# Performance work log

Hardware: AMD Instinct MI355X
Metric: run time of the kernel (lower is better)

Reference implementation:

```python
import jax, jax.numpy as jnp
import numpy as np

D_IN = 128      # NODE/EDGE_EMBEDDING_SIZE
FC_HID = 512    # FC_HIDDEN_SIZE
FEAT = 256      # GNN_FEAT_SIZE
N1 = 2000; E1 = 2000; N2 = 2000; E2 = 2000
GNN_LAYERS = 3
ALPHA = 200.0   # NORM_ALPHA
BS_ITERS = 10   # BS_ITER_NUM
BS_EPS = 1e-4   # BS_EPSILON


def _l2norm(x, axis=-1, eps=1e-12):
    # torch F.normalize(p=2): x / max(||x||, eps)
    n = jnp.sqrt(jnp.sum(x * x, axis=axis, keepdims=True))
    return x / jnp.maximum(n, eps)


def _pairwise_sim(x, y):
    # s = 1 - cdist(x,y,p=2)/max  on batched [B,N,D],[B,M,D]
    x2 = jnp.sum(x * x, axis=-1)[:, :, None]
    y2 = jnp.sum(y * y, axis=-1)[:, None, :]
    d2 = jnp.maximum(x2 + y2 - 2.0 * jnp.einsum('bnd,bmd->bnm', x, y), 0.0)
    dist = jnp.sqrt(d2)
    return 1.0 - dist / jnp.max(dist)


def _gconv(A, x, w_a, b_a, w_u, b_u):
    # A: [B,N,N]; F.normalize(A, p=1, dim=-2) = column L1 normalization
    An = A / jnp.maximum(jnp.sum(jnp.abs(A), axis=-2, keepdims=True), 1e-12)
    ax = jax.nn.relu(x @ w_a + b_a)
    ux = jax.nn.relu(x @ w_u + b_u)
    return jnp.einsum('bnm,bmd->bnd', An, ax) + ux


def _affinity(X, Y, A):
    S = (A + A.T) * 0.5
    return jnp.einsum('bnd,de,bme->bnm', X, S, Y)


def _sinkhorn(s, n1, n2):
    # nrows/ncols equal full dims in Net.forward, so masks are full blocks.
    NT1, NT2 = s.shape[1], s.shape[2]
    r = jnp.arange(NT1)[:, None]
    c = jnp.arange(NT2)[None, :]
    block = ((r < n1) & (c < n2)) | ((r >= n1) & (c >= n2))
    s = (s + BS_EPS) * block[None].astype(s.dtype)
    for i in range(BS_ITERS):
        if i % 2 == 1:
            s = s / jnp.sum(s, axis=2, keepdims=True)  # row normalization
        else:
            s = s / jnp.sum(s, axis=1, keepdims=True)  # column normalization
    return s


def setup_inputs() -> dict:
    key = jax.random.key(0)
    ks = jax.random.split(key, 22)
    f32 = jnp.float32
    def lin_w(k, din, dout):
        return jax.random.uniform(k, (din, dout), dtype=f32,
                                  minval=-1.0, maxval=1.0) / np.sqrt(din)
    stdv = 1.0 / np.sqrt(FEAT)
    inp = {
        'emb1': jax.random.normal(ks[0], (1, N1, D_IN), dtype=f32),
        'emb2': jax.random.normal(ks[1], (1, N2, D_IN), dtype=f32),
        'edge_emb1': jax.random.normal(ks[2], (1, E1, D_IN), dtype=f32),
        'edge_emb2': jax.random.normal(ks[3], (1, E2, D_IN), dtype=f32),
        'Aidx_src': jax.random.uniform(ks[4], (1, N1 + E1, N1 + E1), dtype=f32),
        'Aidx_tgt': jax.random.uniform(ks[5], (1, N2 + E2, N2 + E2), dtype=f32),
        'fc1n_w': lin_w(ks[6], D_IN, FC_HID), 'fc1n_b': jnp.zeros((FC_HID,), f32),
        'fc2n_w': lin_w(ks[7], FC_HID, FEAT), 'fc2n_b': jnp.zeros((FEAT,), f32),
        'fc1e_w': lin_w(ks[8], D_IN, FC_HID), 'fc1e_b': jnp.zeros((FC_HID,), f32),
        'fc2e_w': lin_w(ks[9], FC_HID, FEAT), 'fc2e_b': jnp.zeros((FEAT,), f32),
        'gnn_a_w': jnp.stack([lin_w(k, FEAT, FEAT) for k in jax.random.split(ks[10], GNN_LAYERS)]),
        'gnn_a_b': jnp.zeros((GNN_LAYERS, FEAT), f32),
        'gnn_u_w': jnp.stack([lin_w(k, FEAT, FEAT) for k in jax.random.split(ks[11], GNN_LAYERS)]),
        'gnn_u_b': jnp.zeros((GNN_LAYERS, FEAT), f32),
        'aff_A': jax.random.uniform(ks[12], (GNN_LAYERS, FEAT, FEAT), dtype=f32,
                                    minval=-stdv, maxval=stdv) + jnp.eye(FEAT, dtype=f32),
        'cg_w': lin_w(ks[13], 2 * FEAT, FEAT), 'cg_b': jnp.zeros((FEAT,), f32),
    }
    return inp


def reference(emb1, emb2, edge_emb1, edge_emb2, Aidx_src, Aidx_tgt,
              fc1n_w, fc1n_b, fc2n_w, fc2n_b, fc1e_w, fc1e_b, fc2e_w, fc2e_b,
              gnn_a_w, gnn_a_b, gnn_u_w, gnn_u_b, aff_A, cg_w, cg_b):
    # node embeddings
    h1 = jax.nn.relu(emb1[0] @ fc1n_w + fc1n_b)
    e1n = _l2norm(h1 @ fc2n_w + fc2n_b)[None]            # [1,N1,FEAT]
    h2 = jax.nn.relu(emb2[0] @ fc1n_w + fc1n_b)
    e2n = _l2norm(h2 @ fc2n_w + fc2n_b)[None]            # [1,N2,FEAT]
    Kp = _pairwise_sim(e1n, e2n)
    # edge embeddings
    g1 = jax.nn.relu(edge_emb1[0] @ fc1e_w + fc1e_b)
    e1e = jax.nn.sigmoid(g1 @ fc2e_w + fc2e_b)[None]     # [1,E1,FEAT]
    g2 = jax.nn.relu(edge_emb2[0] @ fc1e_w + fc1e_b)
    e2e = jax.nn.sigmoid(g2 @ fc2e_w + fc2e_b)[None]     # [1,E2,FEAT]
    Ke = _pairwise_sim(e1e, e2e)

    n1, n2 = e1n.shape[1], e2n.shape[1]
    x1 = jnp.concatenate([e1n, e1e], axis=1)             # [1,N1+E1,FEAT]
    x2 = jnp.concatenate([e2n, e2e], axis=1)
    NT1, NT2 = x1.shape[1], x2.shape[1]

    s = None
    for i in range(GNN_LAYERS):
        x1 = _l2norm(_gconv(Aidx_src, x1, gnn_a_w[i], gnn_a_b[i], gnn_u_w[i], gnn_u_b[i]))
        x2 = _l2norm(_gconv(Aidx_tgt, x2, gnn_a_w[i], gnn_a_b[i], gnn_u_w[i], gnn_u_b[i]))
        s = jnp.zeros((1, NT1, NT2), dtype=x1.dtype)
        s = s.at[:, :n1, :n2].set(_affinity(x1[:, :n1], x2[:, :n2], aff_A[i]))
        s = s.at[:, n1:, n2:].set(_affinity(x1[:, n1:], x2[:, n2:], aff_A[i]))
        s = jax.nn.softmax(ALPHA * s, axis=-1)           # Norm layer
        s = _sinkhorn(s, n1, n2)
        if i == GNN_LAYERS - 2:
            x1n = jnp.concatenate([x1, jnp.einsum('bnm,bmd->bnd', s, x2)], axis=-1) @ cg_w + cg_b
            x2n = jnp.concatenate([x2, jnp.einsum('bnm,bnd->bmd', s, x1)], axis=-1) @ cg_w + cg_b
            x1, x2 = x1n, x2n
    return (s, Kp, Ke)
```

## Files before the change

kernel.cpp:

```cpp
#include <hip/hip_runtime.h>
#include <hip/hip_bf16.h>
#include <math.h>
#include <stdint.h>

typedef __hip_bfloat16 bf16;

#define NN 2000
#define NT 4000
#define FEAT 256
#define FC_HID 512
#define D_IN 128
#define ALPHA_C 200.0f
#define BS_EPS_C 1e-4f
#define SABLK 4000000

__device__ __forceinline__ float ldv_dt(const void* p, size_t i, int dt)
{
    return dt ? __bfloat162float(((const bf16*)p)[i]) : ((const float*)p)[i];
}
__device__ __forceinline__ void stv_dt(void* p, size_t i, float v, int dt)
{
    if (dt) ((bf16*)p)[i] = __float2bfloat16(v);
    else    ((float*)p)[i] = v;
}
__device__ __forceinline__ short f2bf(float f)
{
    bf16 h = __float2bfloat16(f);
    short s; __builtin_memcpy(&s, &h, 2); return s;
}
__device__ __forceinline__ float bfbits2f(uint32_t u16)
{
    uint32_t x = u16 << 16; float f; __builtin_memcpy(&f, &x, 4); return f;
}

__device__ __forceinline__ void swizzle_tiles(int& tx, int& ty, int& tz)
{
    int gx = gridDim.x, gy = gridDim.y, gz = gridDim.z;
    int nwg = gx * gy * gz;
    int flat = ((int)blockIdx.z * gy + (int)blockIdx.y) * gx + (int)blockIdx.x;
    int q = nwg >> 3, r = nwg & 7;
    int xcd = flat & 7, s = flat >> 3;
    int mn = xcd < r ? xcd : r;
    int g = xcd * q + mn + s;
    tx = g % gx;
    int gg = g / gx;
    ty = gg % gy;
    tz = gg / gy;
}

__global__ __launch_bounds__(256) void detect_kernel(const uint32_t* __restrict__ emb,
                                                     int* __restrict__ flag)
{
    int tid = threadIdx.x;
    int cnt = 0;
    for (int i = tid; i < 1024; i += 256) {
        uint32_t e = (emb[i] >> 7) & 0xFF;
        if (e >= 0x30 && e <= 0x44) cnt++;
    }
    for (int o = 32; o; o >>= 1) cnt += __shfl_down(cnt, o);
    __shared__ int red[4];
    if ((tid & 63) == 0) red[tid >> 6] = cnt;
    __syncthreads();
    if (tid == 0) *flag = (red[0] + red[1] + red[2] + red[3] > 512) ? 1 : 0;
}

__global__ void telemetry_kernel(uint32_t* out, uint32_t pattern) { out[0] = pattern; }

// ... 136 lines not shown
                int m = t >> 2;
                int gm = m0 + m;
                short loc[8];
#pragma unroll
                for (int j = 0; j < 8; ++j) {
                    int gkj = gk + j;
                    float v = (hv && gm < M && gkj < K)
                                  ? ((const float*)A)[a_off + (size_t)gkj * lda + gm] : 0.f;
                    loc[j] = f2bf(v);
                }
                *(bf16x8*)&Als[t >> 2][h * LDST + kk] = *(bf16x8*)loc;
            }
            {
                int n = t >> 2;
                int gn = n0 + n;
                short* dst = &Bls[n][h * LDST + kk];
                if (hv && gn < N && gk + 8 <= K) {
                    if (bet) {
                        *(uint4*)dst = *(const uint4*)((const ushort*)B + b_off + (size_t)gn * ldb + gk);
                    } else {
                        const float* p = (const float*)B + b_off + (size_t)gn * ldb + gk;
                        float4 r0 = *(const float4*)p, r1 = *(const float4*)(p + 4);
                        short loc[8];
                        loc[0] = f2bf(r0.x); loc[1] = f2bf(r0.y);
                        loc[2] = f2bf(r0.z); loc[3] = f2bf(r0.w);
                        loc[4] = f2bf(r1.x); loc[5] = f2bf(r1.y);
                        loc[6] = f2bf(r1.z); loc[7] = f2bf(r1.w);
                        *(bf16x8*)dst = *(bf16x8*)loc;
                    }
                } else {
                    short loc[8];
#pragma unroll
                    for (int j = 0; j < 8; ++j) {
                        float v = (hv && gn < N && gk + j < K)
                                      ? ldv_dt(B, b_off + (size_t)gn * ldb + gk + j, bet) : 0.f;
                        loc[j] = f2bf(v);
                    }
                    *(bf16x8*)dst = *(bf16x8*)loc;
                }
            }
        }
        __syncthreads();
#pragma unroll
        for (int h = 0; h < 2; ++h) {
            bf16x8 a = *(const bf16x8*)&Als[w * 16 + l16][h * LDST + quad * 8];
#pragma unroll
            for (int fb = 0; fb < 4; ++fb) {
                bf16x8 b = *(const bf16x8*)&Bls[fb * 16 + l16][h * LDST + quad * 8];
                acc[fb] = __builtin_amdgcn_mfma_f32_16x16x32_bf16(a, b, acc[fb], 0, 0, 0);
            }
        }
        __syncthreads();
    }
    const bool atom = (nz > 1);
#pragma unroll
    for (int fb = 0; fb < 4; ++fb) {
        int gc = n0 + fb * 16 + l16;
        if (gc >= N) continue;
        float bv = (!atom && bias) ? ldv_dt(bias, bias_off + gc, bdt) : 0.f;
#pragma unroll
        for (int r = 0; r < 4; ++r) {
            int gr = m0 + w * 16 + quad * 4 + r;
            if (gr >= M) continue;
            float v = acc[fb][r];
            if (atom) {
                if (rowscale) v *= rowscale[gr];
                atomicAdd(&C[(size_t)gr * ldc + gc], v);
            } else {
                v += bv;
                if (epi == 1) v = fmaxf(v, 0.f);
                else if (epi == 2) v = 1.f / (1.f + expf(-v));
                if (rowscale) v *= rowscale[gr];
                if (addsrc) v += addsrc[(size_t)gr * ldadd + gc];
                C[(size_t)gr * ldc + gc] = v;
            }
        }
    }
}

template <int ATR>
__global__ __launch_bounds__(256) void mfma_gemm2(
    const void* __restrict__ A0, const void* __restrict__ A1, int amode,
    const void* __restrict__ B, int bmode, size_t b_off0, size_t b_off1,
    float* __restrict__ C0, float* __restrict__ C1,
    int M, int N, int K, int lda, int ldb, int ldc,
    const float* __restrict__ rs0, const float* __restrict__ rs1,
    const int* __restrict__ dtp)
{
    __shared__ short Als[64][LDSROW];
    __shared__ short Bls[64][LDSROW];
    const int dtf = *dtp;
    const int aet = amode ? dtf : 0;
    const int bet = (bmode == 2) ? 1 : (bmode == 1 ? dtf : 0);
    const int t = threadIdx.x;
    int bx, by, bz;
    swizzle_tiles(bx, by, bz);
    const int tilesY = (M + 63) >> 6;
    const int half = (by >= tilesY) ? 1 : 0;
    const int m0 = (by - half * tilesY) * 64;
    const int n0 = bx * 64;
    const void* A = half ? A1 : A0;
    float* C = half ? C1 : C0;
    const size_t b_off = half ? b_off1 : b_off0;
    const float* rowscale = half ? rs1 : rs0;
    const int nz = gridDim.z;
    int zlo = 0, zhi = K;
    if (nz > 1) {
// ... 44 lines not shown
                int m = t >> 2;
                int gm = m0 + m;
                short loc[8];
#pragma unroll
                for (int j = 0; j < 8; ++j) {
                    int gkj = gk + j;
                    float v = (hv && gm < M && gkj < K)
                                  ? ((const float*)A)[(size_t)gkj * lda + gm] : 0.f;
                    loc[j] = f2bf(v);
                }
                *(bf16x8*)&Als[t >> 2][h * LDST + kk] = *(bf16x8*)loc;
            }
            {
                int n = t >> 2;
                int gn = n0 + n;
                short* dst = &Bls[n][h * LDST + kk];
                if (hv && gn < N && gk + 8 <= K) {
                    if (bet) {
                        *(uint4*)dst = *(const uint4*)((const ushort*)B + b_off + (size_t)gn * ldb + gk);
                    } else {
                        const float* p = (const float*)B + b_off + (size_t)gn * ldb + gk;
                        float4 r0 = *(const float4*)p, r1 = *(const float4*)(p + 4);
                        short loc[8];
                        loc[0] = f2bf(r0.x); loc[1] = f2bf(r0.y);
                        loc[2] = f2bf(r0.z); loc[3] = f2bf(r0.w);
                        loc[4] = f2bf(r1.x); loc[5] = f2bf(r1.y);
                        loc[6] = f2bf(r1.z); loc[7] = f2bf(r1.w);
                        *(bf16x8*)dst = *(bf16x8*)loc;
                    }
                } else {
                    short loc[8];
#pragma unroll
                    for (int j = 0; j < 8; ++j) {
                        float v = (hv && gn < N && gk + j < K)
                                      ? ldv_dt(B, b_off + (size_t)gn * ldb + gk + j, bet) : 0.f;
                        loc[j] = f2bf(v);
                    }
                    *(bf16x8*)dst = *(bf16x8*)loc;
                }
            }
        }
        __syncthreads();
#pragma unroll
        for (int h = 0; h < 2; ++h) {
            bf16x8 a = *(const bf16x8*)&Als[w * 16 + l16][h * LDST + quad * 8];
#pragma unroll
            for (int fb = 0; fb < 4; ++fb) {
                bf16x8 b = *(const bf16x8*)&Bls[fb * 16 + l16][h * LDST + quad * 8];
                acc[fb] = __builtin_amdgcn_mfma_f32_16x16x32_bf16(a, b, acc[fb], 0, 0, 0);
            }
        }
        __syncthreads();
    }
    const bool atom = (nz > 1);
#pragma unroll
    for (int fb = 0; fb < 4; ++fb) {
        int gc = n0 + fb * 16 + l16;
        if (gc >= N) continue;
#pragma unroll
        for (int r = 0; r < 4; ++r) {
            int gr = m0 + w * 16 + quad * 4 + r;
            if (gr >= M) continue;
            float v = acc[fb][r];
            if (rowscale) v *= rowscale[gr];
            if (atom) atomicAdd(&C[(size_t)gr * ldc + gc], v);
            else      C[(size_t)gr * ldc + gc] = v;
        }
    }
}

__global__ __launch_bounds__(256) void mfma_gemm_split(
    const float* __restrict__ A, const float* __restrict__ B, float* __restrict__ C,
    int M, int N, int K)
{
    __shared__ short Ahi[64][LDST];
    __shared__ short Alo[64][LDST];
    __shared__ short Bhi[64][LDST];
    __shared__ short Blo[64][LDST];
    const int t = threadIdx.x;
    int bx, by, bz;
    swizzle_tiles(bx, by, bz);
    const int m0 = by * 64;
    const int n0 = bx * 64;
    const int w = t >> 6, lane = t & 63, quad = lane >> 4, l16 = lane & 15;

    floatx4 acc[4] = {};

    for (int k0 = 0; k0 < K; k0 += 32) {
        {
            int r = t >> 2, kk = (t & 3) * 8;
            int gm = m0 + r, gk = k0 + kk;
            float v[8] = {};
            if (gm < M) {
                const float* p = A + (size_t)gm * K + gk;
                float4 r0 = *(const float4*)p, r1 = *(const float4*)(p + 4);
                v[0] = r0.x; v[1] = r0.y; v[2] = r0.z; v[3] = r0.w;
                v[4] = r1.x; v[5] = r1.y; v[6] = r1.z; v[7] = r1.w;
            }
            short lh[8], ll[8];
#pragma unroll
            for (int j = 0; j < 8; ++j) {
                short h = f2bf(v[j]);
                lh[j] = h;
                ll[j] = f2bf(v[j] - bfbits2f((uint32_t)(uint16_t)h));
            }
            *(bf16x8*)&Ahi[r][kk] = *(bf16x8*)lh;
            *(bf16x8*)&Alo[r][kk] = *(bf16x8*)ll;
        }
        {
            int r = t >> 2, kk = (t & 3) * 8;
            int gn = n0 + r, gk = k0 + kk;
            float v[8] = {};
            if (gn < N) {
                const float* p = B + (size_t)gn * K + gk;
                float4 r0 = *(const float4*)p, r1 = *(const float4*)(p + 4);
                v[0] = r0.x; v[1] = r0.y; v[2] = r0.z; v[3] = r0.w;
                v[4] = r1.x; v[5] = r1.y; v[6] = r1.z; v[7] = r1.w;
            }
            short lh[8], ll[8];
#pragma unroll
            for (int j = 0; j < 8; ++j) {
                short h = f2bf(v[j]);
                lh[j] = h;
                ll[j] = f2bf(v[j] - bfbits2f((uint32_t)(uint16_t)h));
            }
            *(bf16x8*)&Bhi[r][kk] = *(bf16x8*)lh;
            *(bf16x8*)&Blo[r][kk] = *(bf16x8*)ll;
        }
        __syncthreads();
        bf16x8 ah = *(const bf16x8*)&Ahi[w * 16 + l16][quad * 8];
        bf16x8 al = *(const bf16x8*)&Alo[w * 16 + l16][quad * 8];
#pragma unroll
        for (int fb = 0; fb < 4; ++fb) {
            bf16x8 bh = *(const bf16x8*)&Bhi[fb * 16 + l16][quad * 8];
            bf16x8 bl = *(const bf16x8*)&Blo[fb * 16 + l16][quad * 8];
            acc[fb] = __builtin_amdgcn_mfma_f32_16x16x32_bf16(ah, bh, acc[fb], 0, 0, 0);
            acc[fb] = __builtin_amdgcn_mfma_f32_16x16x32_bf16(al, bh, acc[fb], 0, 0, 0);
            acc[fb] = __builtin_amdgcn_mfma_f32_16x16x32_bf16(ah, bl, acc[fb], 0, 0, 0);
        }
        __syncthreads();
    }
#pragma unroll
    for (int fb = 0; fb < 4; ++fb) {
        int gc = n0 + fb * 16 + l16;
        if (gc >= N) continue;
#pragma unroll
        for (int r = 0; r < 4; ++r) {
            int gr = m0 + w * 16 + quad * 4 + r;
            if (gr >= M) continue;
            C[(size_t)gr * N + gc] = acc[fb][r];
        }
    }
}

__global__ __launch_bounds__(256) void mfma_mlp_split(
    const void* __restrict__ A, int amode,
    const short* __restrict__ Whi, const short* __restrict__ Wlo,
    float* __restrict__ C, int M, int N, int K, int ldc,
    const void* __restrict__ bias, int epi, const int* __restrict__ dtp)
{
    __shared__ short Ahi[64][LDST];
    __shared__ short Alo[64][LDST];
    __shared__ short Bh[64][LDST];
    __shared__ short Bl[64][LDST];
    const int dtf = *dtp;
    const int aet = amode ? dtf : 0;
    const int t = threadIdx.x;
    int bx, by, bz;
    swizzle_tiles(bx, by, bz);
    const int m0 = by * 64;
    const int n0 = bx * 64;
    const int w = t >> 6, lane = t & 63, quad = lane >> 4, l16 = lane & 15;

    floatx4 acc[4] = {};

    for (int k0 = 0; k0 < K; k0 += 32) {
        {
            int r = t >> 2, kk = (t & 3) * 8;
            int gm = m0 + r, gk = k0 + kk;
            float v[8] = {};
            if (gm < M) {
                if (aet) {
                    uint4 raw = *(const uint4*)((const ushort*)A + (size_t)gm * K + gk);
                    uint32_t uu[4] = {raw.x, raw.y, raw.z, raw.w};
#pragma unroll
                    for (int q = 0; q < 4; ++q) {
                        v[2 * q]     = bfbits2f(uu[q] & 0xFFFFu);
                        v[2 * q + 1] = bfbits2f(uu[q] >> 16);
                    }
                } else {
                    const float* p = (const float*)A + (size_t)gm * K + gk;
                    float4 r0 = *(const float4*)p, r1 = *(const float4*)(p + 4);
                    v[0] = r0.x; v[1] = r0.y; v[2] = r0.z; v[3] = r0.w;
                    v[4] = r1.x; v[5] = r1.y; v[6] = r1.z; v[7] = r1.w;
                }
            }
            short lh[8], ll[8];
#pragma unroll
            for (int j = 0; j < 8; ++j) {
                short h = f2bf(v[j]);
                lh[j] = h;
                ll[j] = f2bf(v[j] - bfbits2f((uint32_t)(uint16_t)h));
            }
            *(bf16x8*)&Ahi[r][kk] = *(bf16x8*)lh;
            *(bf16x8*)&Alo[r][kk] = *(bf16x8*)ll;
        }
        {
            int n = t >> 2, kk = (t & 3) * 8;
            int gn = n0 + n, gk = k0 + kk;
            if (gn < N) {
                *(uint4*)&Bh[n][kk] = *(const uint4*)&Whi[(size_t)gn * K + gk];
                *(uint4*)&Bl[n][kk] = *(const uint4*)&Wlo[(size_t)gn * K + gk];
            } else {
                short z[8] = {};
                *(bf16x8*)&Bh[n][kk] = *(bf16x8*)z;
                *(bf16x8*)&Bl[n][kk] = *(bf16x8*)z;
            }
        }
        __syncthreads();
        bf16x8 ah = *(const bf16x8*)&Ahi[w * 16 + l16][quad * 8];
        bf16x8 al = *(const bf16x8*)&Alo[w * 16 + l16][quad * 8];
#pragma unroll
        for (int fb = 0; fb < 4; ++fb) {
            bf16x8 bh = *(const bf16x8*)&Bh[fb * 16 + l16][quad * 8];
// ... 5 lines not shown
        __syncthreads();
    }
#pragma unroll
    for (int fb = 0; fb < 4; ++fb) {
        int gc = n0 + fb * 16 + l16;
        if (gc >= N) continue;
        float bv = bias ? ldv_dt(bias, gc, *dtp) : 0.f;
#pragma unroll
        for (int r = 0; r < 4; ++r) {
            int gr = m0 + w * 16 + quad * 4 + r;
            if (gr >= M) continue;
            float v = acc[fb][r] + bv;
            if (epi == 1) v = fmaxf(v, 0.f);
            else if (epi == 2) v = 1.f / (1.f + expf(-v));
            C[(size_t)gr * ldc + gc] = v;
        }
    }
}

__global__ void fill_kernel(float* p, float v, int n)
{
    int i = blockIdx.x * 256 + threadIdx.x;
    if (i < n) p[i] = v;
}

__global__ __launch_bounds__(256) void l2norm_kernel(const float* __restrict__ src,
                                                     int lds, float* __restrict__ dst)
{
    int row = blockIdx.x, tid = threadIdx.x;
    float v = src[(size_t)row * lds + tid];
    float s = v * v;
    for (int o = 32; o; o >>= 1) s += __shfl_down(s, o);
    __shared__ float red[4];
    if ((tid & 63) == 0) red[tid >> 6] = s;
    __syncthreads();
    float tot = red[0] + red[1] + red[2] + red[3];
    float scale = 1.f / fmaxf(sqrtf(tot), 1e-12f);
    dst[(size_t)row * FEAT + tid] = v * scale;
}

__global__ __launch_bounds__(256) void rownorm2_kernel(const float* __restrict__ src,
                                                       float* __restrict__ out)
{
    int row = blockIdx.x, tid = threadIdx.x;
    float v = src[(size_t)row * FEAT + tid];
    float s = v * v;
    for (int o = 32; o; o >>= 1) s += __shfl_down(s, o);
    __shared__ float red[4];
    if ((tid & 63) == 0) red[tid >> 6] = s;
    __syncthreads();
    if (tid == 0) out[row] = red[0] + red[1] + red[2] + red[3];
}

__global__ __launch_bounds__(256) void d2max_rows_kernel(const float* __restrict__ G,
                                                         const float* __restrict__ x2,
                                                         const float* __restrict__ y2,
                                                         float* __restrict__ rowmax)
{
    int i = blockIdx.x, tid = threadIdx.x;
    float xi = x2[i];
    const float* Gr = G + (size_t)i * NN;
    float m = 0.f;
    for (int j = tid; j < NN; j += 256)
        m = fmaxf(m, xi + y2[j] - 2.f * Gr[j]);
    for (int o = 32; o; o >>= 1) m = fmaxf(m, __shfl_down(m, o));
    __shared__ float red[4];
    if ((tid & 63) == 0) red[tid >> 6] = m;
    __syncthreads();
    if (tid == 0) rowmax[i] = fmaxf(fmaxf(red[0], red[1]), fmaxf(red[2], red[3]));
}

__global__ __launch_bounds__(256) void maxreduce_kernel(const float* __restrict__ rowmax,
                                                        float* __restrict__ gmax, int n)
{
    int tid = threadIdx.x;
    float m = 0.f;
    for (int i = tid; i < n; i += 256) m = fmaxf(m, rowmax[i]);
    for (int o = 32; o; o >>= 1) m = fmaxf(m, __shfl_down(m, o));
    __shared__ float red[4];
    if ((tid & 63) == 0) red[tid >> 6] = m;
    __syncthreads();
    if (tid == 0) *gmax = sqrtf(fmaxf(fmaxf(fmaxf(red[0], red[1]),
                                            fmaxf(red[2], red[3])), 0.f));
}

__global__ __launch_bounds__(256) void pw_out_kernel(void* __restrict__ out, size_t elem_off,
                                                     const float* __restrict__ G,
                                                     const float* __restrict__ x2,
                                                     const float* __restrict__ y2,
                                                     const float* __restrict__ gmax,
                                                     const int* __restrict__ dtp)
{
    int j = blockIdx.x * 256 + threadIdx.x;
    int i = blockIdx.y;
    if (j >= NN) return;
    float inv = 1.f / *gmax;
    float d2 = fmaxf(x2[i] + y2[j] - 2.f * G[(size_t)i * NN + j], 0.f);
    stv_dt(out, elem_off + (size_t)i * NN + j, 1.f - sqrtf(d2) * inv, *dtp);
}

__global__ __launch_bounds__(256) void colsum_kernel(const void* __restrict__ A0,
                                                     const void* __restrict__ A1,
                                                     float* __restrict__ out,
                                                     const int* __restrict__ dtp)
{
    const void* A = blockIdx.z ? A1 : A0;
    int dt = *dtp;
    int col = blockIdx.x * 256 + threadIdx.x;
    if (col >= NT) return;
    int r0 = blockIdx.y * 100;
    float s = 0.f;
#pragma unroll 4
    for (int r = r0; r < r0 + 100; ++r) s += fabsf(ldv_dt(A, (size_t)r * NT + col, dt));
    atomicAdd(&out[blockIdx.z * NT + col], s);
}

__global__ void recipclamp_kernel(float* p, int n)
{
    int i = blockIdx.x * 256 + threadIdx.x;
    if (i < n) p[i] = 1.f / fmaxf(p[i], 1e-12f);
}

__global__ __launch_bounds__(256) void symavg_kernel(const void* __restrict__ A,
                                                     size_t a_off,
                                                     float* __restrict__ S,
                                                     const int* __restrict__ dtp)
{
    int dt = *dtp;
    int i = blockIdx.x, j = threadIdx.x;
    S[i * 256 + j] = 0.5f * (ldv_dt(A, a_off + i * 256 + j, dt) +
                             ldv_dt(A, a_off + j * 256 + i, dt));
}

__global__ __launch_bounds__(256) void softmax_stats_kernel(const float* __restrict__ Sa,
                                                            float* __restrict__ ms,
                                                            float* __restrict__ dinv)
{
    int row = blockIdx.x, z = blockIdx.z, tid = threadIdx.x;
    const float* Srow = Sa + (size_t)z * SABLK + (size_t)row * NN;
    __shared__ float red[4];
    float m = 0.f;
    for (int j = tid; j < NN; j += 256) m = fmaxf(m, ALPHA_C * Srow[j]);
    for (int o = 32; o; o >>= 1) m = fmaxf(m, __shfl_down(m, o));
    if ((tid & 63) == 0) red[tid >> 6] = m;
    __syncthreads();
    m = fmaxf(fmaxf(red[0], red[1]), fmaxf(red[2], red[3]));
    __syncthreads();
    float s = 0.f;
    for (int j = tid; j < NN; j += 256) s += expf(ALPHA_C * Srow[j] - m);
    for (int o = 32; o; o >>= 1) s += __shfl_down(s, o);
// ... 64 lines not shown
}

__global__ __launch_bounds__(256) void writes_kernel(void* __restrict__ out,
                                                     const float* __restrict__ E,
                                                     const float* __restrict__ rvec,
                                                     const float* __restrict__ cvec,
                                                     const int* __restrict__ dtp)
{
    int i = blockIdx.x, tid = threadIdx.x;
    int dt = *dtp;
    int z = (i < NN) ? 0 : 1;
    int r = z ? i - NN : i;
    const float* Erow = E + (size_t)z * SABLK + (size_t)r * NN;
    float rv = rvec[i];
    for (int j = tid; j < NT; j += 256) {
        float v = 0.f;
        bool inblk = z ? (j >= NN) : (j < NN);
        if (inblk) {
            int jj = z ? (j - NN) : j;
            v = rv * Erow[jj] * cvec[j];
            if (!(v == v) || fabsf(v) > 1e30f) v = 0.f;
        }
        stv_dt(out, (size_t)i * NT + j, v, dt);
    }
}

extern "C" void kernel_launch(void* const* d_in, const int* in_sizes, int n_in,
                              void* d_out, int out_size, void* d_ws, size_t ws_size,
                              hipStream_t stream)
{
    (void)in_sizes; (void)n_in; (void)out_size;
    const void* emb1   = d_in[0];
    const void* emb2   = d_in[1];
    const void* eemb1  = d_in[2];
    const void* eemb2  = d_in[3];
    const void* Asrc   = d_in[4];
    const void* Atgt   = d_in[5];
    const void* fc1n_w = d_in[6];
    const void* fc1n_b = d_in[7];
    const void* fc2n_w = d_in[8];
    const void* fc2n_b = d_in[9];
    const void* fc1e_w = d_in[10];
    const void* fc1e_b = d_in[11];
    const void* fc2e_w = d_in[12];
    const void* fc2e_b = d_in[13];
    const void* gnn_a_w = d_in[14];
    const void* gnn_a_b = d_in[15];
    const void* gnn_u_w = d_in[16];
    const void* gnn_u_b = d_in[17];
    const void* aff_A  = d_in[18];
    const void* cg_w   = d_in[19];
    const void* cg_b   = d_in[20];

    const size_t KP_OFF = 16000000;
    const size_t KE_OFF = 20000000;

    const size_t NEED = 50808960;
    if (ws_size < NEED) {
        float tv = 10000.f + (float)(ws_size >> 20);
        bf16 tb = __float2bfloat16(tv);
        uint16_t tbits; __builtin_memcpy(&tbits, &tb, 2);
        uint32_t pattern = ((uint32_t)tbits << 16) | tbits;
        telemetry_kernel<<<1, 1, 0, stream>>>((uint32_t*)d_out, pattern);
        return;
    }
    char* Wb = (char*)d_ws;
    size_t off = 0;
    auto allocf = [&](size_t n) { float* p = (float*)(Wb + off); off += n * 4; return p; };
    float* x1     = allocf(1024000);
    float* x2     = allocf(1024000);
    float* ax     = allocf(1024000);
    float* ux     = allocf(1024000);
    float* XS     = allocf(512000);
    float* Ssym   = allocf(65536);
    float* colsum = allocf(8192);
    float* rn2a   = allocf(2048);
    float* rn2b   = allocf(2048);
    float* rvec   = allocf(4096);
    float* cvec   = allocf(4096);
    float* ms     = allocf(4096);
    float* dinv   = allocf(4096);
    float* gmax   = allocf(16);
    int*   dtp    = (int*)allocf(16);
    float* Sa     = allocf(8000000);
    float* G      = Sa;
    float* tmpx1  = Sa;
    float* tmpx2  = Sa + 1024000;
    float* h      = ax;
    float* partial = XS;
    float* XS2    = ax;
    short* wuT    = (short*)(Sa + 2100000);
    float* bias512 = Sa + 2200000;
    float* axu_b  = Sa + 2300000;
    short* axT_b  = (short*)(Sa + 6450000);
    short* cgT    = (short*)Ssym;
    short* XST    = (short*)XS;
    short* w1hiT = (short*)Sa;
    short* w1loT = w1hiT + FC_HID * D_IN;
    short* w2hiT = w1loT + FC_HID * D_IN;
    short* w2loT = w2hiT + FEAT * FC_HID;

    dim3 B(256);
    auto g2 = [](int M, int N) { return dim3((N + 63) / 64, (M + 63) / 64); };
    auto gb2 = [](int Mh, int N, int nz) {
        return dim3((N + 63) / 64, 2 * ((Mh + 63) / 64), nz);
    };
    auto gt = [](int R, int C) { return dim3((C + 63) / 64, (R + 63) / 64); };
    const float* NF = nullptr;
    const void* NV = nullptr;

    detect_kernel<<<1, B, 0, stream>>>((const uint32_t*)emb1, dtp);

    struct { const void* e; const void* w1; const void* b1; const void* w2;
             const void* b2; float* dst; int epi; } mlp[4] = {
        {emb1,  fc1n_w, fc1n_b, fc2n_w, fc2n_b, x1,          0},
        {emb2,  fc1n_w, fc1n_b, fc2n_w, fc2n_b, x2,          0},
        {eemb1, fc1e_w, fc1e_b, fc2e_w, fc2e_b, x1 + 512000, 2},
        {eemb2, fc1e_w, fc1e_b, fc2e_w, fc2e_b, x2 + 512000, 2},
    };
    for (int m = 0; m < 4; ++m) {
        if (m == 0 || m == 2) {
            transpose_split_kernel<<<gt(D_IN, FC_HID), B, 0, stream>>>(
                mlp[m].w1, 1, 0, w1hiT, w1loT, D_IN, FC_HID, dtp);
            transpose_split_kernel<<<gt(FC_HID, FEAT), B, 0, stream>>>(
                mlp[m].w2, 1, 0, w2hiT, w2loT, FC_HID, FEAT, dtp);
        }
        mfma_mlp_split<<<g2(NN, FC_HID), B, 0, stream>>>(
            mlp[m].e, 1, w1hiT, w1loT, h, NN, FC_HID, D_IN, FC_HID,
            mlp[m].b1, 1, dtp);
        mfma_mlp_split<<<g2(NN, FEAT), B, 0, stream>>>(
            h, 0, w2hiT, w2loT, mlp[m].dst, NN, FEAT, FC_HID, FEAT,
            mlp[m].b2, mlp[m].epi, dtp);
        if (mlp[m].epi == 0)
            l2norm_kernel<<<NN, B, 0, stream>>>(mlp[m].dst, FEAT, mlp[m].dst);
    }

    for (int e = 0; e < 2; ++e) {
        const float* a = e ? x1 + 512000 : x1;
        const float* b = e ? x2 + 512000 : x2;
        size_t oeo = e ? KE_OFF : KP_OFF;
        rownorm2_kernel<<<NN, B, 0, stream>>>(a, rn2a);
        rownorm2_kernel<<<NN, B, 0, stream>>>(b, rn2b);
        mfma_gemm_split<<<g2(NN, NN), B, 0, stream>>>(a, b, G, NN, NN, FEAT);
        d2max_rows_kernel<<<NN, B, 0, stream>>>(G, rn2a, rn2b, partial);
        maxreduce_kernel<<<1, B, 0, stream>>>(partial, gmax, NN);
        pw_out_kernel<<<dim3(8, NN), B, 0, stream>>>(d_out, oeo, G, rn2a, rn2b, gmax, dtp);
    }

    fill_kernel<<<(8192 + 255) / 256, B, 0, stream>>>(colsum, 0.f, 8192);
    colsum_kernel<<<dim3(16, 40, 2), B, 0, stream>>>(Asrc, Atgt, colsum, dtp);
    recipclamp_kernel<<<(8000 + 255) / 256, B, 0, stream>>>(colsum, 8000);

    float* src1 = x1;
    for (int i = 0; i < 3; ++i) {
        size_t wo = (size_t)i * 65536, bo = (size_t)i * 256;
        transpose_bf16_kernel<<<gt(256, 256), B, 0, stream>>>(
            gnn_a_w, 1, wo, wuT, 256, 256, 256, NF, dtp);
        transpose_bf16_kernel<<<gt(256, 256), B, 0, stream>>>(
            gnn_u_w, 1, wo, wuT + 65536, 256, 256, 256, NF, dtp);
        concat_bias_kernel<<<1, B, 0, stream>>>(gnn_a_b, gnn_u_b, bo, bias512, dtp);
        mfma_gemm<0><<<g2(2 * NT, 512), B, 0, stream>>>(
            src1, 0, 0, wuT, 2, 0, axu_b, 2 * NT, 512, FEAT, FEAT, FEAT, 512,
            bias512, 0, 0, NF, NF, 0, 1, dtp);
        transpose_bf16_kernel<<<gt(2 * NT, 256), B, 0, stream>>>(
            axu_b, 0, 0, axT_b, 2 * NT, 256, 512, colsum, dtp);
        mfma_gemm2<0><<<gb2(NT, FEAT, 8), B, 0, stream>>>(
            Asrc, Atgt, 1, axT_b, 2, 0, NT,
            axu_b + 256, axu_b + (size_t)NT * 512 + 256,
            NT, FEAT, NT, NT, 2 * NT, 512, NF, NF, dtp);
        l2norm_kernel<<<2 * NT, B, 0, stream>>>(axu_b + 256, 512, x1);
        src1 = x1;
        if (i >= 1) {
            symavg_kernel<<<256, B, 0, stream>>>(aff_A, (size_t)i * 65536, Ssym, dtp);
            mfma_gemm<0><<<g2(2 * NN, FEAT), B, 0, stream>>>(
                x1, 0, 0, Ssym, 0, 0, XS2, 2 * NN, FEAT, FEAT, FEAT, FEAT, FEAT,
                NV, 0, 0, NF, NF, 0, 0, dtp);
            mfma_gemm2<0><<<gb2(NN, NN, 1), B, 0, stream>>>(
                XS2, XS2 + 512000, 0, x2, 0, 0, 512000,
                Sa, Sa + SABLK, NN, NN, FEAT, FEAT, FEAT, NN, NF, NF, dtp);
            softmax_stats_kernel<<<dim3(NN, 1, 2), B, 0, stream>>>(Sa, ms, dinv);
            exp_transform_kernel<<<dim3(2, NN, 2), B, 0, stream>>>(Sa, ms, dinv);
            for (int t = 0; t < 10; ++t) {
                if ((t & 1) == 0) {
                    fill_kernel<<<16, B, 0, stream>>>(partial, 0.f, 4096);
                    colmv_partial_kernel<<<dim3(8, 40, 2), B, 0, stream>>>(
                        Sa, t == 0 ? NF : rvec, partial);
                    recip_vec_kernel<<<16, B, 0, stream>>>(partial, cvec, 4000);
                } else {
                    rowmv_kernel<<<dim3(NN, 1, 2), B, 0, stream>>>(Sa, cvec, rvec);
                }
            }
            if (i == 1) {
                fill_kernel<<<8000, B, 0, stream>>>(ax, 0.f, 2048000);
                transpose_bf16_kernel<<<gt(2 * NN, 256), B, 0, stream>>>(
                    x2, 0, 0, XST, 2 * NN, 256, 256, cvec, dtp);
                mfma_gemm2<0><<<gb2(NN, FEAT, 8), B, 0, stream>>>(
                    Sa, Sa + SABLK, 0, XST, 2, 0, NN,
                    ax, ax + 512000, NN, FEAT, NN, NN, 2 * NN, FEAT,
                    rvec, rvec + NN, dtp);
                transpose_bf16_kernel<<<gt(2 * NN, 256), B, 0, stream>>>(
                    x1, 0, 0, XST, 2 * NN, 256, 256, rvec, dtp);
                mfma_gemm2<1><<<gb2(NN, FEAT, 8), B, 0, stream>>>(
                    Sa, Sa + SABLK, 0, XST, 2, 0, NN,
                    ux, ux + 512000, NN, FEAT, NN, NN, 2 * NN, FEAT,
                    cvec, cvec + NN, dtp);
                transpose_bf16_kernel<<<gt(512, 256), B, 0, stream>>>(
                    cg_w, 1, 0, cgT, 512, 256, 256, NF, dtp);
                mfma_gemm<0><<<g2(2 * NT, FEAT), B, 0, stream>>>(
                    x1, 0, 0, cgT, 2, 0, tmpx1, 2 * NT, FEAT, FEAT, FEAT, 512, FEAT,
                    cg_b, 0, 1, NF, NF, 0, 0, dtp);
                mfma_gemm<0><<<g2(2 * NT, FEAT), B, 0, stream>>>(
                    ax, 0, 0, cgT, 2, 256, tmpx1, 2 * NT, FEAT, FEAT, FEAT, 512, FEAT,
                    NV, 0, 0, NF, tmpx1, FEAT, 0, dtp);
                src1 = tmpx1;
            }
            if (i == 2) {
                writes_kernel<<<NT, B, 0, stream>>>(d_out, Sa, rvec, cvec, dtp);
            }
        }
    }
}
```

Measured before the change: 1.425 ms.

## Use 128x128 MFMA tiles for aggregation GEMMs and batch paired preprocessing launches

Adds a 128x128-tile variant of the paired GEMM, with each wave computing a 64x64 sub-tile, and uses it for the large A·X aggregation and S·X cross-graph products. This raises data reuse per loaded LDS tile. It also merges the MLP and pairwise-similarity stages for the two graphs into single launches using a half/z index, which roughly halves the number of launches in the prologue. The larger tiles use more registers and produce fewer blocks, which could reduce occupancy.

After: 1.448 ms. No clear change (+1.6%).

```diff
diff --git a/kernel.cpp b/kernel.cpp
--- a/kernel.cpp
+++ b/kernel.cpp
@@ -13,6 +13,8 @@
 #define ALPHA_C 200.0f
 #define BS_EPS_C 1e-4f
 #define SABLK 4000000
+#define KP_OFF_C 16000000
+#define KE_OFF_C 20000000
 
 __device__ __forceinline__ float ldv_dt(const void* p, size_t i, int dt)
 {
@@ -255,7 +257,7 @@
         }
         __syncthreads();
     }
-    const bool atom = (nz > 1);
+    const bool atom = (gridDim.z > 1);
 #pragma unroll
     for (int fb = 0; fb < 4; ++fb) {
         int gc = n0 + fb * 16 + l16;
@@ -406,7 +408,7 @@
         }
         __syncthreads();
     }
-    const bool atom = (nz > 1);
+    const bool atom = (gridDim.z > 1);
 #pragma unroll
     for (int fb = 0; fb < 4; ++fb) {
         int gc = n0 + fb * 16 + l16;
@@ -423,8 +425,157 @@
     }
 }
 
-__global__ __launch_bounds__(256) void mfma_gemm_split(
-    const float* __restrict__ A, const float* __restrict__ B, float* __restrict__ C,
+template <int ATR>
+__global__ __launch_bounds__(256) void mfma_gemm2_128(
+    const void* __restrict__ A0, const void* __restrict__ A1, int amode,
+    const void* __restrict__ B, int bmode, size_t b_off0, size_t b_off1,
+    float* __restrict__ C0, float* __restrict__ C1,
+    int M, int N, int K, int lda, int ldb, int ldc,
+    const float* __restrict__ rs0, const float* __restrict__ rs1,
+    const int* __restrict__ dtp)
+{
+    __shared__ short Als[128][LDST];
+    __shared__ short Bls[128][LDST];
+    const int dtf = *dtp;
+    const int aet = amode ? dtf : 0;
+    const int bet = (bmode == 2) ? 1 : (bmode == 1 ? dtf : 0);
+    const int t = threadIdx.x;
+    int bx, by, bz;
+    swizzle_tiles(bx, by, bz);
+    const int tilesY = (M + 127) >> 7;
+    const int half = (by >= tilesY) ? 1 : 0;
+    const int m0 = (by - half * tilesY) * 128;
+    const int n0 = bx * 128;
+    const void* A = half ? A1 : A0;
+    float* C = half ? C1 : C0;
+    const size_t b_off = half ? b_off1 : b_off0;
+    const float* rowscale = half ? rs1 : rs0;
+    const int nz = gridDim.z;
+    int zlo = 0, zhi = K;
+    if (nz > 1) {
+        int kb = ((K + nz * 32 - 1) / (nz * 32)) * 32;
+        zlo = bz * kb;
+        zhi = zlo + kb < K ? zlo + kb : K;
+        if (zlo > K) zlo = K;
+    }
+    const int w = t >> 6, lane = t & 63, quad = lane >> 4, l16 = lane & 15;
+    const int wr = w >> 1, wc = w & 1;
+
+    floatx4 acc[4][4] = {};
+
+    for (int k0 = zlo; k0 < zhi; k0 += 32) {
+#pragma unroll
+        for (int it = 0; it < 2; ++it) {
+            int chunk = t + it * 256;
+            int row = chunk >> 2;
+            int kkc = (chunk & 3) * 8;
+            int gk = k0 + kkc;
+            {
+                int gm = m0 + row;
+                short* dst = &Als[row][kkc];
+                if (ATR == 0) {
+                    if (gm < M && gk + 8 <= K) {
+                        if (aet) {
+                            *(uint4*)dst = *(const uint4*)((const ushort*)A + (size_t)gm * lda + gk);
+                        } else {
+                            const float* p = (const float*)A + (size_t)gm * lda + gk;
+                            float4 r0 = *(const float4*)p, r1 = *(const float4*)(p + 4);
+                            short loc[8];
+                            loc[0] = f2bf(r0.x); loc[1] = f2bf(r0.y);
+                            loc[2] = f2bf(r0.z); loc[3] = f2bf(r0.w);
+                            loc[4] = f2bf(r1.x); loc[5] = f2bf(r1.y);
+                            loc[6] = f2bf(r1.z); loc[7] = f2bf(r1.w);
+                            *(bf16x8*)dst = *(bf16x8*)loc;
+                        }
+                    } else {
+                        short loc[8];
+#pragma unroll
+                        for (int j = 0; j < 8; ++j) {
+                            float v = 0.f;
+                            if (gm < M && gk + j < K)
+                                v = ldv_dt(A, (size_t)gm * lda + gk + j, aet);
+                            loc[j] = f2bf(v);
+                        }
+                        *(bf16x8*)dst = *(bf16x8*)loc;
+                    }
+                } else {
+                    short loc[8];
+#pragma unroll
+                    for (int j = 0; j < 8; ++j) {
+                        int gkj = gk + j;
+                        float v = (gm < M && gkj < K)
+                                      ? ((const float*)A)[(size_t)gkj * lda + gm] : 0.f;
+                        loc[j] = f2bf(v);
+                    }
+                    *(bf16x8*)dst = *(bf16x8*)loc;
+                }
+            }
+            {
+                int gn = n0 + row;
+                short* dst = &Bls[row][kkc];
+                if (gn < N && gk + 8 <= K) {
+                    if (bet) {
+                        *(uint4*)dst = *(const uint4*)((const ushort*)B + b_off + (size_t)gn * ldb + gk);
+                    } else {
+                        const float* p = (const float*)B + b_off + (size_t)gn * ldb + gk;
+                        float4 r0 = *(const float4*)p, r1 = *(const float4*)(p + 4);
+                        short loc[8];
+                        loc[0] = f2bf(r0.x); loc[1] = f2bf(r0.y);
+                        loc[2] = f2bf(r0.z); loc[3] = f2bf(r0.w);
+                        loc[4] = f2bf(r1.x); loc[5] = f2bf(r1.y);
+                        loc[6] = f2bf(r1.z); loc[7] = f2bf(r1.w);
+                        *(bf16x8*)dst = *(bf16x8*)loc;
+                    }
+                } else {
+                    short loc[8];
+#pragma unroll
+                    for (int j = 0; j < 8; ++j) {
+                        float v = (gn < N && gk + j < K)
+                                      ? ldv_dt(B, b_off + (size_t)gn * ldb + gk + j, bet) : 0.f;
+                        loc[j] = f2bf(v);
+                    }
+                    *(bf16x8*)dst = *(bf16x8*)loc;
+                }
+            }
+        }
+        __syncthreads();
+        bf16x8 a[4];
+#pragma unroll
+        for (int r = 0; r < 4; ++r)
+            a[r] = *(const bf16x8*)&Als[wr * 64 + r * 16 + l16][quad * 8];
+#pragma unroll
+        for (int c = 0; c < 4; ++c) {
+            bf16x8 b = *(const bf16x8*)&Bls[wc * 64 + c * 16 + l16][quad * 8];
+#pragma unroll
+            for (int r = 0; r < 4; ++r)
+                acc[r][c] = __builtin_amdgcn_mfma_f32_16x16x32_bf16(a[r], b, acc[r][c], 0, 0, 0);
+        }
+        __syncthreads();
+    }
+    const bool atom = (gridDim.z > 1);
+#pragma unroll
+    for (int c = 0; c < 4; ++c) {
+        int gc = n0 + wc * 64 + c * 16 + l16;
+        if (gc >= N) continue;
+#pragma unroll
+        for (int r = 0; r < 4; ++r) {
+#pragma unroll
+            for (int rr = 0; rr < 4; ++rr) {
+                int gr = m0 + wr * 64 + r * 16 + quad * 4 + rr;
+                if (gr >= M) continue;
+                float v = acc[r][c][rr];
+                if (rowscale) v *= rowscale[gr];
+                if (atom) atomicAdd(&C[(size_t)gr * ldc + gc], v);
+                else      C[(size_t)gr * ldc + gc] = v;
+            }
+        }
+    }
+}
+
+__global__ __launch_bounds__(256) void mfma_gemm_split2(
+    const float* __restrict__ A0, const float* __restrict__ A1,
+    const float* __restrict__ B0, const float* __restrict__ B1,
+    float* __restrict__ C0, float* __restrict__ C1,
     int M, int N, int K)
 {
     __shared__ short Ahi[64][LDST];
@@ -434,8 +585,13 @@
     const int t = threadIdx.x;
     int bx, by, bz;
     swizzle_tiles(bx, by, bz);
-    const int m0 = by * 64;
+    const int tilesY = (M + 63) >> 6;
+    const int half = (by >= tilesY) ? 1 : 0;
+    const int m0 = (by - half * tilesY) * 64;
     const int n0 = bx * 64;
+    const float* A = half ? A1 : A0;
+    const float* Bp = half ? B1 : B0;
+    float* C = half ? C1 : C0;
     const int w = t >> 6, lane = t & 63, quad = lane >> 4, l16 = lane & 15;
 
     floatx4 acc[4] = {};
@@ -466,7 +622,7 @@
             int gn = n0 + r, gk = k0 + kk;
             float v[8] = {};
             if (gn < N) {
-                const float* p = B + (size_t)gn * K + gk;
+                const float* p = Bp + (size_t)gn * K + gk;
                 float4 r0 = *(const float4*)p, r1 = *(const float4*)(p + 4);
                 v[0] = r0.x; v[1] = r0.y; v[2] = r0.z; v[3] = r0.w;
                 v[4] = r1.x; v[5] = r1.y; v[6] = r1.z; v[7] = r1.w;
@@ -507,10 +663,11 @@
     }
 }
 
-__global__ __launch_bounds__(256) void mfma_mlp_split(
-    const void* __restrict__ A, int amode,
+__global__ __launch_bounds__(256) void mfma_mlp_split2(
+    const void* __restrict__ A0, const void* __restrict__ A1, int amode,
     const short* __restrict__ Whi, const short* __restrict__ Wlo,
-    float* __restrict__ C, int M, int N, int K, int ldc,
+    float* __restrict__ C0, float* __restrict__ C1,
+    int M, int N, int K, int ldc,
     const void* __restrict__ bias, int epi, const int* __restrict__ dtp)
 {
     __shared__ short Ahi[64][LDST];
@@ -522,8 +679,12 @@
     const int t = threadIdx.x;
     int bx, by, bz;
     swizzle_tiles(bx, by, bz);
-    const int m0 = by * 64;
+    const int tilesY = (M + 63) >> 6;
+    const int half = (by >= tilesY) ? 1 : 0;
+    const int m0 = (by - half * tilesY) * 64;
     const int n0 = bx * 64;
+    const void* A = half ? A1 : A0;
+    float* C = half ? C1 : C0;
     const int w = t >> 6, lane = t & 63, quad = lane >> 4, l16 = lane & 15;
 
     floatx4 acc[4] = {};
@@ -635,13 +796,15 @@
     if (tid == 0) out[row] = red[0] + red[1] + red[2] + red[3];
 }
 
-__global__ __launch_bounds__(256) void d2max_rows_kernel(const float* __restrict__ G,
-                                                         const float* __restrict__ x2,
-                                                         const float* __restrict__ y2,
+__global__ __launch_bounds__(256) void d2max_rows_kernel(const float* __restrict__ Gb,
+                                                         const float* __restrict__ rnA,
+                                                         const float* __restrict__ rnB,
                                                          float* __restrict__ rowmax)
 {
-    int i = blockIdx.x, tid = threadIdx.x;
-    float xi = x2[i];
+    int i = blockIdx.x, z = blockIdx.z, tid = threadIdx.x;
+    const float* G = Gb + (size_t)z * SABLK;
+    float xi = rnA[z * NN + i];
+    const float* y2 = rnB + z * NN;
     const float* Gr = G + (size_t)i * NN;
     float m = 0.f;
     for (int j = tid; j < NN; j += 256)
@@ -650,35 +813,38 @@
     __shared__ float red[4];
     if ((tid & 63) == 0) red[tid >> 6] = m;
     __syncthreads();
-    if (tid == 0) rowmax[i] = fmaxf(fmaxf(red[0], red[1]), fmaxf(red[2], red[3]));
+    if (tid == 0) rowmax[z * 2048 + i] = fmaxf(fmaxf(red[0], red[1]), fmaxf(red[2], red[3]));
 }
 
 __global__ __launch_bounds__(256) void maxreduce_kernel(const float* __restrict__ rowmax,
                                                         float* __restrict__ gmax, int n)
 {
-    int tid = threadIdx.x;
+    int tid = threadIdx.x, z = blockIdx.z;
+    const float* rm = rowmax + z * 2048;
     float m = 0.f;
-    for (int i = tid; i < n; i += 256) m = fmaxf(m, rowmax[i]);
+    for (int i = tid; i < n; i += 256) m = fmaxf(m, rm[i]);
     for (int o = 32; o; o >>= 1) m = fmaxf(m, __shfl_down(m, o));
     __shared__ float red[4];
     if ((tid & 63) == 0) red[tid >> 6] = m;
     __syncthreads();
-    if (tid == 0) *gmax = sqrtf(fmaxf(fmaxf(fmaxf(red[0], red[1]),
-                                            fmaxf(red[2], red[3])), 0.f));
-}
-
-__global__ __launch_bounds__(256) void pw_out_kernel(void* __restrict__ out, size_t elem_off,
-                                                     const float* __restrict__ G,
-                                                     const float* __restrict__ x2,
-                                                     const float* __restrict__ y2,
+    if (tid == 0) gmax[z] = sqrtf(fmaxf(fmaxf(fmaxf(red[0], red[1]),
+                                              fmaxf(red[2], red[3])), 0.f));
+}
+
+__global__ __launch_bounds__(256) void pw_out_kernel(void* __restrict__ out,
+                                                     const float* __restrict__ Gb,
+                                                     const float* __restrict__ rnA,
+                                                     const float* __restrict__ rnB,
                                                      const float* __restrict__ gmax,
                                                      const int* __restrict__ dtp)
 {
     int j = blockIdx.x * 256 + threadIdx.x;
-    int i = blockIdx.y;
+    int i = blockIdx.y, z = blockIdx.z;
     if (j >= NN) return;
-    float inv = 1.f / *gmax;
-    float d2 = fmaxf(x2[i] + y2[j] - 2.f * G[(size_t)i * NN + j], 0.f);
+    size_t elem_off = z ? KE_OFF_C : KP_OFF_C;
+    const float* G = Gb + (size_t)z * SABLK;
+    float inv = 1.f / gmax[z];
+    float d2 = fmaxf(rnA[z * NN + i] + rnB[z * NN + j] - 2.f * G[(size_t)i * NN + j], 0.f);
     stv_dt(out, elem_off + (size_t)i * NN + j, 1.f - sqrtf(d2) * inv, *dtp);
 }
 
@@ -849,9 +1015,6 @@
     const void* cg_w   = d_in[19];
     const void* cg_b   = d_in[20];
 
-    const size_t KP_OFF = 16000000;
-    const size_t KE_OFF = 20000000;
-
     const size_t NEED = 50808960;
     if (ws_size < NEED) {
         float tv = 10000.f + (float)(ws_size >> 20);
@@ -880,10 +1043,8 @@
     float* gmax   = allocf(16);
     int*   dtp    = (int*)allocf(16);
     float* Sa     = allocf(8000000);
-    float* G      = Sa;
     float* tmpx1  = Sa;
     float* tmpx2  = Sa + 1024000;
-    float* h      = ax;
     float* partial = XS;
     float* XS2    = ax;
     short* wuT    = (short*)(Sa + 2100000);
@@ -902,47 +1063,44 @@
     auto gb2 = [](int Mh, int N, int nz) {
         return dim3((N + 63) / 64, 2 * ((Mh + 63) / 64), nz);
     };
+    auto gb128 = [](int Mh, int N, int nz) {
+        return dim3((N + 127) / 128, 2 * ((Mh + 127) / 128), nz);
+    };
     auto gt = [](int R, int C) { return dim3((C + 63) / 64, (R + 63) / 64); };
     const float* NF = nullptr;
     const void* NV = nullptr;
 
     detect_kernel<<<1, B, 0, stream>>>((const uint32_t*)emb1, dtp);
 
-    struct { const void* e; const void* w1; const void* b1; const void* w2;
-             const void* b2; float* dst; int epi; } mlp[4] = {
-        {emb1,  fc1n_w, fc1n_b, fc2n_w, fc2n_b, x1,          0},
-        {emb2,  fc1n_w, fc1n_b, fc2n_w, fc2n_b, x2,          0},
-        {eemb1, fc1e_w, fc1e_b, fc2e_w, fc2e_b, x1 + 512000, 2},
-        {eemb2, fc1e_w, fc1e_b, fc2e_w, fc2e_b, x2 + 512000, 2},
+    struct { const void* e0; const void* e1; const void* w1; const void* b1;
+             const void* w2; const void* b2; float* d0; float* d1; int epi; } mp[2] = {
+        {emb1,  emb2,  fc1n_w, fc1n_b, fc2n_w, fc2n_b, x1,          x2,          0},
+        {eemb1, eemb2, fc1e_w, fc1e_b, fc2e_w, fc2e_b, x1 + 512000, x2 + 512000, 2},
     };
-    for (int m = 0; m < 4; ++m) {
-        if (m == 0 || m == 2) {
-            transpose_split_kernel<<<gt(D_IN, FC_HID), B, 0, stream>>>(
-                mlp[m].w1, 1, 0, w1hiT, w1loT, D_IN, FC_HID, dtp);
-            transpose_split_kernel<<<gt(FC_HID, FEAT), B, 0, stream>>>(
-                mlp[m].w2, 1, 0, w2hiT, w2loT, FC_HID, FEAT, dtp);
-        }
-        mfma_mlp_split<<<g2(NN, FC_HID), B, 0, stream>>>(
-            mlp[m].e, 1, w1hiT, w1loT, h, NN, FC_HID, D_IN, FC_HID,
-            mlp[m].b1, 1, dtp);
-        mfma_mlp_split<<<g2(NN, FEAT), B, 0, stream>>>(
-            h, 0, w2hiT, w2loT, mlp[m].dst, NN, FEAT, FC_HID, FEAT,
-            mlp[m].b2, mlp[m].epi, dtp);
-        if (mlp[m].epi == 0)
-            l2norm_kernel<<<NN, B, 0, stream>>>(mlp[m].dst, FEAT, mlp[m].dst);
-    }
-
-    for (int e = 0; e < 2; ++e) {
-        const float* a = e ? x1 + 512000 : x1;
-        const float* b = e ? x2 + 512000 : x2;
-        size_t oeo = e ? KE_OFF : KP_OFF;
-        rownorm2_kernel<<<NN, B, 0, stream>>>(a, rn2a);
-        rownorm2_kernel<<<NN, B, 0, stream>>>(b, rn2b);
-        mfma_gemm_split<<<g2(NN, NN), B, 0, stream>>>(a, b, G, NN, NN, FEAT);
-        d2max_rows_kernel<<<NN, B, 0, stream>>>(G, rn2a, rn2b, partial);
-        maxreduce_kernel<<<1, B, 0, stream>>>(partial, gmax, NN);
-        pw_out_kernel<<<dim3(8, NN), B, 0, stream>>>(d_out, oeo, G, rn2a, rn2b, gmax, dtp);
-    }
+    for (int p = 0; p < 2; ++p) {
+        transpose_split_kernel<<<gt(D_IN, FC_HID), B, 0, stream>>>(
+            mp[p].w1, 1, 0, w1hiT, w1loT, D_IN, FC_HID, dtp);
+        transpose_split_kernel<<<gt(FC_HID, FEAT), B, 0, stream>>>(
+            mp[p].w2, 1, 0, w2hiT, w2loT, FC_HID, FEAT, dtp);
+        mfma_mlp_split2<<<gb2(NN, FC_HID, 1), B, 0, stream>>>(
+            mp[p].e0, mp[p].e1, 1, w1hiT, w1loT, ax, ax + 1024000,
+            NN, FC_HID, D_IN, FC_HID, mp[p].b1, 1, dtp);
+        mfma_mlp_split2<<<gb2(NN, FEAT, 1), B, 0, stream>>>(
+            ax, ax + 1024000, 0, w2hiT, w2loT, mp[p].d0, mp[p].d1,
+            NN, FEAT, FC_HID, FEAT, mp[p].b2, mp[p].epi, dtp);
+        if (mp[p].epi == 0) {
+            l2norm_kernel<<<NN, B, 0, stream>>>(mp[p].d0, FEAT, mp[p].d0);
+            l2norm_kernel<<<NN, B, 0, stream>>>(mp[p].d1, FEAT, mp[p].d1);
+        }
+    }
+
+    rownorm2_kernel<<<2 * NN, B, 0, stream>>>(x1, rvec);
+    rownorm2_kernel<<<2 * NN, B, 0, stream>>>(x2, cvec);
+    mfma_gemm_split2<<<gb2(NN, NN, 1), B, 0, stream>>>(
+        x1, x1 + 512000, x2, x2 + 512000, Sa, Sa + SABLK, NN, NN, FEAT);
+    d2max_rows_kernel<<<dim3(NN, 1, 2), B, 0, stream>>>(Sa, rvec, cvec, partial);
+    maxreduce_kernel<<<dim3(1, 1, 2), B, 0, stream>>>(partial, gmax, NN);
+    pw_out_kernel<<<dim3(8, NN, 2), B, 0, stream>>>(d_out, Sa, rvec, cvec, gmax, dtp);
 
     fill_kernel<<<(8192 + 255) / 256, B, 0, stream>>>(colsum, 0.f, 8192);
     colsum_kernel<<<dim3(16, 40, 2), B, 0, stream>>>(Asrc, Atgt, colsum, dtp);
@@ -961,7 +1119,7 @@
             bias512, 0, 0, NF, NF, 0, 1, dtp);
         transpose_bf16_kernel<<<gt(2 * NT, 256), B, 0, stream>>>(
             axu_b, 0, 0, axT_b, 2 * NT, 256, 512, colsum, dtp);
-        mfma_gemm2<0><<<gb2(NT, FEAT, 8), B, 0, stream>>>(
+        mfma_gemm2_128<0><<<gb128(NT, FEAT, 8), B, 0, stream>>>(
             Asrc, Atgt, 1, axT_b, 2, 0, NT,
             axu_b + 256, axu_b + (size_t)NT * 512 + 256,
             NT, FEAT, NT, NT, 2 * NT, 512, NF, NF, dtp);
@@ -991,13 +1149,13 @@
                 fill_kernel<<<8000, B, 0, stream>>>(ax, 0.f, 2048000);
                 transpose_bf16_kernel<<<gt(2 * NN, 256), B, 0, stream>>>(
                     x2, 0, 0, XST, 2 * NN, 256, 256, cvec, dtp);
-                mfma_gemm2<0><<<gb2(NN, FEAT, 8), B, 0, stream>>>(
+                mfma_gemm2_128<0><<<gb128(NN, FEAT, 8), B, 0, stream>>>(
                     Sa, Sa + SABLK, 0, XST, 2, 0, NN,
                     ax, ax + 512000, NN, FEAT, NN, NN, 2 * NN, FEAT,
                     rvec, rvec + NN, dtp);
                 transpose_bf16_kernel<<<gt(2 * NN, 256), B, 0, stream>>>(
                     x1, 0, 0, XST, 2 * NN, 256, 256, rvec, dtp);
-                mfma_gemm2<1><<<gb2(NN, FEAT, 8), B, 0, stream>>>(
+                mfma_gemm2_128<1><<<gb128(NN, FEAT, 8), B, 0, stream>>>(
                     Sa, Sa + SABLK, 0, XST, 2, 0, NN,
                     ux, ux + 512000, NN, FEAT, NN, NN, 2 * NN, FEAT,
                     cvec, cvec + NN, dtp);
@@ -1016,4 +1174,5 @@
             }
         }
     }
-}
+    (void)rn2a; (void)rn2b; (void)tmpx2;
+}
```
